# Kernel tuning notes

Measured on AMD Instinct MI355X. Metric: run time of the kernel, lower is better.

## Reference

```python
import jax, jax.numpy as jnp
import numpy as np

B = 512          # batch
V = 6890         # SMPL vertices
NB = 10          # num_betas
NJ = 24          # joints (root + 23 body)
# canonical SMPL kinematic tree (parents[0] = -1 for root)
PARENTS = np.array([-1,0,0,0,1,2,3,4,5,6,7,8,9,9,9,12,13,14,16,17,18,19,20,21], dtype=np.int32)


def rodrigues(rot_vecs):
    """Axis-angle [N,3] -> rotation matrices [N,3,3] (matches batch_rodrigues)."""
    angle = jnp.linalg.norm(rot_vecs + 1e-8, axis=1, keepdims=True)  # [N,1]
    rot_dir = rot_vecs / angle
    cos = jnp.cos(angle)[:, :, None]  # [N,1,1]
    sin = jnp.sin(angle)[:, :, None]
    rx, ry, rz = rot_dir[:, 0], rot_dir[:, 1], rot_dir[:, 2]
    zeros = jnp.zeros_like(rx)
    K = jnp.stack([zeros, -rz, ry,
                   rz, zeros, -rx,
                   -ry, rx, zeros], axis=1).reshape(-1, 3, 3)
    I = jnp.eye(3, dtype=rot_vecs.dtype)
    return I[None] + sin * K + (1.0 - cos) * jnp.matmul(K, K)


def setup_inputs() -> dict:
    key = jax.random.key(0)
    ks = jax.random.split(key, 8)
    betas = jnp.concatenate([jnp.ones((B, 1), jnp.float32),
                             0.5 * jax.random.normal(ks[0], (B, NB), jnp.float32)], axis=1)
    body_pose = 0.3 * jax.random.normal(ks[1], (B, 3 * (NJ - 1)), jnp.float32)
    global_orient = 0.3 * jax.random.normal(ks[2], (B, 3), jnp.float32)
    transl = jax.random.normal(ks[3], (B, 3), jnp.float32)
    shapedirs = 0.01 * jax.random.normal(ks[4], (V, 3, NB), jnp.float32)
    v_template = jax.random.normal(ks[5], (V, 3), jnp.float32)
    Jr = jax.random.uniform(ks[6], (NJ, V), jnp.float32)
    Jr = Jr / jnp.sum(Jr, axis=1, keepdims=True)
    W = jax.random.uniform(ks[7], (V, NJ), jnp.float32)
    W = W / jnp.sum(W, axis=1, keepdims=True)             # convex skinning weights
    return dict(betas=betas, body_pose=body_pose, global_orient=global_orient,
                transl=transl, shapedirs=shapedirs, v_template=v_template,
                J_regressor=Jr, lbs_weights=W)


def reference(betas, body_pose, global_orient, transl,
              shapedirs, v_template, J_regressor, lbs_weights):
    dt = v_template.dtype
    blend = jnp.einsum('bl,mkl->bmk', betas[:, 1:], shapedirs)            # [B,V,3]
    v_shaped = (v_template[None] + blend) * betas[:, 0][:, None, None]    # [B,V,3]
    J = jnp.einsum('bik,ji->bjk', v_shaped, J_regressor)                  # [B,NJ,3]
    # ---- updatePose: axis-angle -> rotmats
    full_pose = jnp.concatenate([global_orient, body_pose], axis=1)       # [B,NJ*3]
    rot_mats = rodrigues(full_pose.reshape(-1, 3)).reshape(-1, NJ, 3, 3)  # [B,NJ,3,3]
    # ---- kinematic chain (batch_rigid_transform)
    rel = J.at[:, 1:].add(-J[:, PARENTS[1:]])                             # rel joint offsets
    T_local = jnp.concatenate([rot_mats, rel[..., None]], axis=3)         # [B,NJ,3,4]
    bottom = jnp.broadcast_to(jnp.array([0, 0, 0, 1], dt), (rot_mats.shape[0], NJ, 1, 4))
    T_local = jnp.concatenate([T_local, bottom], axis=2)                  # [B,NJ,4,4]
    chain = [T_local[:, 0]]
    for i in range(1, NJ):  # fixed 24-node tree
        chain.append(jnp.matmul(chain[PARENTS[i]], T_local[:, i]))
    transforms = jnp.stack(chain, axis=1)                                 # [B,NJ,4,4]
    J_transformed = transforms[:, :, :3, 3]                               # [B,NJ,3]
    # relative transforms: subtract rotated rest joint from translation column
    init_t = jnp.einsum('bnij,bnj->bni', transforms[:, :, :3, :3], J)
    A = transforms.at[:, :, :3, 3].add(-init_t)                           # [B,NJ,4,4]
    # ---- skinning: T = W @ A, apply to homogeneous verts
    T = jnp.einsum('vn,bnij->bvij', lbs_weights, A)                       # [B,V,4,4]
    verts = (jnp.einsum('bvij,bvj->bvi', T[:, :, :3, :3], v_shaped)
             + T[:, :, :3, 3] + transl[:, None])                          # [B,V,3]
    return verts, J_transformed
```

## Files before the change

### kernel.cpp

```cpp
#include <hip/hip_runtime.h>

#define BATCH 512
#define V 6890
#define NJ 24
#define VH (V/2)

#define SD_N (V*30)
#define VT_N (V*3)
#define W_N  (V*24)
#define TOT_PK (SD_N+VT_N+W_N)

#define A_OFF   0
#define BS_OFF  147456
#define JT_OFF  155648
#define JS_OFF  155720
#define PK_OFF  156672

__device__ const int d_par[NJ] = {-1,0,0,0,1,2,3,4,5,6,7,8,9,9,9,12,13,14,16,17,18,19,20,21};

__global__ __launch_bounds__(256) void prep_k(
    const float* __restrict__ sd, const float* __restrict__ vt, const float* __restrict__ W,
    float* __restrict__ dst)
{
  int i = blockIdx.x*256 + threadIdx.x;
  if (i >= TOT_PK) return;
  float val;
  if (i < SD_N){ int j=i/V, v=i-j*V; val = sd[v*30+j]; }
  else if (i < SD_N+VT_N){ int o=i-SD_N; int j=o/V, v=o-j*V; val = vt[v*3+j]; }
  else { int o=i-SD_N-VT_N; int j=o/V, v=o-j*V; val = W[v*24+j]; }
  dst[i] = val;
}

__global__ __launch_bounds__(256) void jreg_k(
    const float* __restrict__ Jr, const float* __restrict__ pk,
    float* __restrict__ JTo, float* __restrict__ JSo)
{
  const int j = blockIdx.x;
  const int c = blockIdx.y;
  const int t = threadIdx.x;
  const float* __restrict__ col = (c<3) ? (pk + (30+c)*V) : (pk + (c-3)*V);
  float acc = 0.f;
  for (int v=t; v<V; v+=256){
    acc = fmaf(Jr[j*V+v], col[v], acc);
  }
  __shared__ float red[256];
  red[t]=acc; __syncthreads();
  for (int s=128;s>0;s>>=1){ if(t<s) red[t]+=red[t+s]; __syncthreads(); }
  if (t==0){
    if (c<3) JTo[j*3+c]=red[0];
    else {
      int idx=c-3, k=idx/10, l=idx-10*(idx/10);
      JSo[(j*3+k)*10+l] = red[0];
    }
  }
}

__global__ __launch_bounds__(64) void batch_k(
    const float* __restrict__ betas, const float* __restrict__ body_pose,
    const float* __restrict__ go, const float* __restrict__ transl,
    const float* __restrict__ JT, const float* __restrict__ JS,
    float* __restrict__ A, float* __restrict__ bsc, float* __restrict__ jout)
{
  const int b = blockIdx.x;
  const int t = threadIdx.x;
  __shared__ float lb[11];
  __shared__ float lJ[72];
  __shared__ float lR[NJ*9];
  __shared__ float lL[NJ*12];
  __shared__ float lW[NJ*12];
  if (t < 11) lb[t] = betas[b*11+t];
  __syncthreads();
  const float b0 = lb[0];
  for (int idx=t; idx<72; idx+=64){
    float s = JT[idx];
    #pragma unroll
    for (int l=0;l<10;l++) s = fmaf(lb[1+l], JS[idx*10+l], s);
    lJ[idx] = b0*s;
  }
  if (t==0) bsc[b*16] = b0;
  if (t>=1 && t<11) bsc[b*16+t] = b0*lb[t];
  if (t<3) bsc[b*16+11+t] = transl[b*3+t];
  if (t < NJ){
    float p0,p1,p2;
    if (t==0){ p0=go[b*3+0]; p1=go[b*3+1]; p2=go[b*3+2]; }
    else { int o=b*69+(t-1)*3; p0=body_pose[o]; p1=body_pose[o+1]; p2=body_pose[o+2]; }
    float a0=p0+1e-8f, a1=p1+1e-8f, a2=p2+1e-8f;
    float angle = sqrtf(a0*a0+a1*a1+a2*a2);
    float inv = 1.0f/angle;
    float rx=p0*inv, ry=p1*inv, rz=p2*inv;
    float sn = sinf(angle), cs = cosf(angle), mc = 1.0f-cs;
    float K[9] = {0.f,-rz,ry, rz,0.f,-rx, -ry,rx,0.f};
    float KK[9];
    #pragma unroll
    for (int r=0;r<3;r++)
      #pragma unroll
      for (int c=0;c<3;c++)
        KK[r*3+c] = K[r*3+0]*K[0+c] + K[r*3+1]*K[3+c] + K[r*3+2]*K[6+c];
    #pragma unroll
    for (int e=0;e<9;e++){
      float ident = (e==0||e==4||e==8)?1.0f:0.0f;
      lR[t*9+e] = ident + sn*K[e] + mc*KK[e];
    }
  }
  __syncthreads();
  for (int idx=t; idx<288; idx+=64){
    int j = idx/12, rc = idx-12*j, r = rc>>2, c = rc&3;
    float val;
    if (c<3) val = lR[j*9 + r*3 + c];
    else {
      int p = (j==0) ? 0 : d_par[j];
      val = (j==0) ? lJ[r] : (lJ[j*3+r] - lJ[p*3+r]);
    }
    lL[idx] = val;
  }
  __syncthreads();
  if (t<12) lW[t] = lL[t];
  __syncthreads();
  for (int i=1;i<NJ;i++){
    if (t<12){
      int p = d_par[i];
      int r = t>>2, c = t&3;
      float s = lW[p*12+r*4+0]*lL[i*12+0+c]
              + lW[p*12+r*4+1]*lL[i*12+4+c]
              + lW[p*12+r*4+2]*lL[i*12+8+c];
      if (c==3) s += lW[p*12+r*4+3];
      lW[i*12+t] = s;
    }
    __syncthreads();
  }
  for (int idx=t; idx<72; idx+=64){
    int j=idx/3, k=idx-3*j;
    jout[b*72+idx] = lW[j*12+k*4+3];
  }
  const int g = b>>2, q = b&3;
  float* __restrict__ Ab = A + g*1152 + q*12;
  for (int idx=t; idx<288; idx+=64){
    int n=idx/12, rc=idx-12*n, r=rc>>2, c=rc&3;
    float val = lW[n*12+rc];
    if (c==3){
      val -= lW[n*12+r*4+0]*lJ[n*3+0] + lW[n*12+r*4+1]*lJ[n*3+1] + lW[n*12+r*4+2]*lJ[n*3+2];
    }
    Ab[n*48 + rc] = val;
  }
}

__global__ __launch_bounds__(256) void main_k(
    const float* __restrict__ A, const float* __restrict__ bsc,
    const float2* __restrict__ pk, float* __restrict__ out)
{
  const int vh = blockIdx.x*256 + threadIdx.x;
  if (vh >= VH) return;
  const int bg = blockIdx.y;
  const float* __restrict__ Ag = A + bg*1152;
  const float* __restrict__ bs = bsc + bg*64;

  const float2 vt0 = pk[30*VH + vh];
  const float2 vt1 = pk[31*VH + vh];
  const float2 vt2 = pk[32*VH + vh];

  float2 vs[4][3];
#pragma unroll
  for (int q=0;q<4;q++){
    const float b0 = bs[q*16];
    vs[q][0] = make_float2(b0*vt0.x, b0*vt0.y);
    vs[q][1] = make_float2(b0*vt1.x, b0*vt1.y);
    vs[q][2] = make_float2(b0*vt2.x, b0*vt2.y);
  }
#pragma unroll
  for (int l=0;l<10;l++){
    const float2 s0 = pk[(0*10+l)*VH + vh];
    const float2 s1 = pk[(1*10+l)*VH + vh];
    const float2 s2 = pk[(2*10+l)*VH + vh];
#pragma unroll
    for (int q=0;q<4;q++){
      const float c = bs[q*16+1+l];
      vs[q][0].x = fmaf(c, s0.x, vs[q][0].x); vs[q][0].y = fmaf(c, s0.y, vs[q][0].y);
      vs[q][1].x = fmaf(c, s1.x, vs[q][1].x); vs[q][1].y = fmaf(c, s1.y, vs[q][1].y);
      vs[q][2].x = fmaf(c, s2.x, vs[q][2].x); vs[q][2].y = fmaf(c, s2.y, vs[q][2].y);
    }
  }

  float y[4][6];
#pragma unroll
  for (int q=0;q<4;q++)
#pragma unroll
    for (int i=0;i<6;i++) y[q][i] = 0.f;

#pragma unroll 4
  for (int n=0;n<NJ;n++){
    const float2 w = pk[(33+n)*VH + vh];
#pragma unroll
    for (int q=0;q<4;q++){
      const float* __restrict__ an = Ag + n*48 + q*12;
      float tt;
      tt = fmaf(an[2], vs[q][2].x, fmaf(an[1], vs[q][1].x, fmaf(an[0], vs[q][0].x, an[3])));
      y[q][0] = fmaf(w.x, tt, y[q][0]);
      tt = fmaf(an[2], vs[q][2].y, fmaf(an[1], vs[q][1].y, fmaf(an[0], vs[q][0].y, an[3])));
      y[q][1] = fmaf(w.y, tt, y[q][1]);
      tt = fmaf(an[6], vs[q][2].x, fmaf(an[5], vs[q][1].x, fmaf(an[4], vs[q][0].x, an[7])));
      y[q][2] = fmaf(w.x, tt, y[q][2]);
      tt = fmaf(an[6], vs[q][2].y, fmaf(an[5], vs[q][1].y, fmaf(an[4], vs[q][0].y, an[7])));
      y[q][3] = fmaf(w.y, tt, y[q][3]);
      tt = fmaf(an[10], vs[q][2].x, fmaf(an[9], vs[q][1].x, fmaf(an[8], vs[q][0].x, an[11])));
      y[q][4] = fmaf(w.x, tt, y[q][4]);
      tt = fmaf(an[10], vs[q][2].y, fmaf(an[9], vs[q][1].y, fmaf(an[8], vs[q][0].y, an[11])));
      y[q][5] = fmaf(w.y, tt, y[q][5]);
    }
  }

  const int v0 = 2*vh;
#pragma unroll
  for (int q=0;q<4;q++){
    const float t0 = bs[q*16+11], t1 = bs[q*16+12], t2 = bs[q*16+13];
    const int b = bg*4 + q;
    float2* __restrict__ o2 = (float2*)(out + (b*V + v0)*3);
    o2[0] = make_float2(y[q][0]+t0, y[q][2]+t1);
    o2[1] = make_float2(y[q][4]+t2, y[q][1]+t0);
    o2[2] = make_float2(y[q][3]+t1, y[q][5]+t2);
  }
}

extern "C" void kernel_launch(void* const* d_in, const int* in_sizes, int n_in,
                              void* d_out, int out_size, void* d_ws, size_t ws_size,
                              hipStream_t stream)
{
  const float* betas     = (const float*)d_in[0];
  const float* body_pose = (const float*)d_in[1];
  const float* go        = (const float*)d_in[2];
  const float* transl    = (const float*)d_in[3];
  const float* sdirs     = (const float*)d_in[4];
  const float* vtempl    = (const float*)d_in[5];
  const float* Jr        = (const float*)d_in[6];
  const float* lw        = (const float*)d_in[7];
  float* wsf = (float*)d_ws;
  float* out = (float*)d_out;

  hipLaunchKernelGGL(prep_k, dim3((TOT_PK+255)/256), dim3(256), 0, stream,
                     sdirs, vtempl, lw, wsf+PK_OFF);
  hipLaunchKernelGGL(jreg_k, dim3(24,33), dim3(256), 0, stream,
                     Jr, wsf+PK_OFF, wsf+JT_OFF, wsf+JS_OFF);
  hipLaunchKernelGGL(batch_k, dim3(BATCH), dim3(64), 0, stream,
                     betas, body_pose, go, transl, wsf+JT_OFF, wsf+JS_OFF,
                     wsf+A_OFF, wsf+BS_OFF, out + BATCH*V*3);
  hipLaunchKernelGGL(main_k, dim3((VH+255)/256, BATCH/4), dim3(256), 0, stream,
                     wsf+A_OFF, wsf+BS_OFF, (const float2*)(wsf+PK_OFF), out);
}
```

Measured before the change: 149.5 us.

## Fuse prep and joint regression, level-parallel kinematic chain, two vertex pairs per thread

Merges the weight-repacking kernel and the joint-regression kernel into one launch, with the regression reading the original strided inputs directly so it no longer waits on the repack. The serial 23-step kinematic chain in batch_k becomes 8 depth levels, where all joints at one level are computed in parallel, cutting barrier count. The main skinning kernel now processes two vertex pairs per thread so the per-joint A coefficients loaded from memory are reused across both. The trade-offs are more registers (possible occupancy loss), half as many blocks in main_k, and strided uncoalesced reads in the regression path.

New measurement: 237.0 us. +58.5%, slower.

```diff
diff --git a/kernel.cpp b/kernel.cpp
--- a/kernel.cpp
+++ b/kernel.cpp
@@ -9,6 +9,7 @@
 #define VT_N (V*3)
 #define W_N  (V*24)
 #define TOT_PK (SD_N+VT_N+W_N)
+#define PREP_BLOCKS ((TOT_PK+255)/256)
 
 #define A_OFF   0
 #define BS_OFF  147456
@@ -17,40 +18,44 @@
 #define PK_OFF  156672
 
 __device__ const int d_par[NJ] = {-1,0,0,0,1,2,3,4,5,6,7,8,9,9,9,12,13,14,16,17,18,19,20,21};
-
-__global__ __launch_bounds__(256) void prep_k(
-    const float* __restrict__ sd, const float* __restrict__ vt, const float* __restrict__ W,
-    float* __restrict__ dst)
-{
-  int i = blockIdx.x*256 + threadIdx.x;
-  if (i >= TOT_PK) return;
-  float val;
-  if (i < SD_N){ int j=i/V, v=i-j*V; val = sd[v*30+j]; }
-  else if (i < SD_N+VT_N){ int o=i-SD_N; int j=o/V, v=o-j*V; val = vt[v*3+j]; }
-  else { int o=i-SD_N-VT_N; int j=o/V, v=o-j*V; val = W[v*24+j]; }
-  dst[i] = val;
-}
-
-__global__ __launch_bounds__(256) void jreg_k(
-    const float* __restrict__ Jr, const float* __restrict__ pk,
-    float* __restrict__ JTo, float* __restrict__ JSo)
-{
-  const int j = blockIdx.x;
-  const int c = blockIdx.y;
+__device__ const int lvlJ[8][5] = {{1,2,3,0,0},{4,5,6,0,0},{7,8,9,0,0},{10,11,12,13,14},
+                                   {15,16,17,0,0},{18,19,0,0,0},{20,21,0,0,0},{22,23,0,0,0}};
+__device__ const int lvlP[8][5] = {{0,0,0,0,0},{1,2,3,0,0},{4,5,6,0,0},{7,8,9,9,9},
+                                   {12,13,14,0,0},{16,17,0,0,0},{18,19,0,0,0},{20,21,0,0,0}};
+__device__ const int lvlN[8] = {3,3,3,5,3,2,2,2};
+
+__global__ __launch_bounds__(256) void prepjr_k(
+    const float* __restrict__ sd, const float* __restrict__ vt,
+    const float* __restrict__ W, const float* __restrict__ Jr,
+    float* __restrict__ dst, float* __restrict__ JTo, float* __restrict__ JSo)
+{
+  const int bx = blockIdx.x;
   const int t = threadIdx.x;
-  const float* __restrict__ col = (c<3) ? (pk + (30+c)*V) : (pk + (c-3)*V);
-  float acc = 0.f;
-  for (int v=t; v<V; v+=256){
-    acc = fmaf(Jr[j*V+v], col[v], acc);
-  }
-  __shared__ float red[256];
-  red[t]=acc; __syncthreads();
-  for (int s=128;s>0;s>>=1){ if(t<s) red[t]+=red[t+s]; __syncthreads(); }
-  if (t==0){
-    if (c<3) JTo[j*3+c]=red[0];
-    else {
-      int idx=c-3, k=idx/10, l=idx-10*(idx/10);
-      JSo[(j*3+k)*10+l] = red[0];
+  if (bx < PREP_BLOCKS){
+    int i = bx*256 + t;
+    if (i >= TOT_PK) return;
+    float val;
+    if (i < SD_N){ int j=i/V, v=i-j*V; val = sd[v*30+j]; }
+    else if (i < SD_N+VT_N){ int o=i-SD_N; int j=o/V, v=o-j*V; val = vt[v*3+j]; }
+    else { int o=i-SD_N-VT_N; int j=o/V, v=o-j*V; val = W[v*24+j]; }
+    dst[i] = val;
+  } else {
+    const int idx = bx - PREP_BLOCKS;
+    const int j = idx/33, c = idx-33*(idx/33);
+    float acc = 0.f;
+    for (int v=t; v<V; v+=256){
+      float x = (c<3) ? vt[v*3+c] : sd[v*30+(c-3)];
+      acc = fmaf(Jr[j*V+v], x, acc);
+    }
+    __shared__ float red[256];
+    red[t]=acc; __syncthreads();
+    for (int s=128;s>0;s>>=1){ if(t<s) red[t]+=red[t+s]; __syncthreads(); }
+    if (t==0){
+      if (c<3) JTo[j*3+c]=red[0];
+      else {
+        int ii=c-3, k=ii/10, l=ii-10*(ii/10);
+        JSo[(j*3+k)*10+l] = red[0];
+      }
     }
   }
 }
@@ -116,15 +121,17 @@
   __syncthreads();
   if (t<12) lW[t] = lL[t];
   __syncthreads();
-  for (int i=1;i<NJ;i++){
-    if (t<12){
-      int p = d_par[i];
-      int r = t>>2, c = t&3;
-      float s = lW[p*12+r*4+0]*lL[i*12+0+c]
-              + lW[p*12+r*4+1]*lL[i*12+4+c]
-              + lW[p*12+r*4+2]*lL[i*12+8+c];
+  #pragma unroll
+  for (int lev=0; lev<8; lev++){
+    const int cnt = lvlN[lev];
+    if (t < cnt*12){
+      int jl = t/12, e = t-12*jl, r = e>>2, c = e&3;
+      int j = lvlJ[lev][jl], p = lvlP[lev][jl];
+      float s = lW[p*12+r*4+0]*lL[j*12+0+c]
+              + lW[p*12+r*4+1]*lL[j*12+4+c]
+              + lW[p*12+r*4+2]*lL[j*12+8+c];
       if (c==3) s += lW[p*12+r*4+3];
-      lW[i*12+t] = s;
+      lW[j*12+e] = s;
     }
     __syncthreads();
   }
@@ -148,75 +155,104 @@
     const float* __restrict__ A, const float* __restrict__ bsc,
     const float2* __restrict__ pk, float* __restrict__ out)
 {
-  const int vh = blockIdx.x*256 + threadIdx.x;
-  if (vh >= VH) return;
+  const int t = threadIdx.x;
+  const int p0 = blockIdx.x*512 + t;
+  if (p0 >= VH) return;
+  const int p1r = p0 + 256;
+  const bool has1 = (p1r < VH);
+  const int p1 = has1 ? p1r : p0;
   const int bg = blockIdx.y;
   const float* __restrict__ Ag = A + bg*1152;
   const float* __restrict__ bs = bsc + bg*64;
 
-  const float2 vt0 = pk[30*VH + vh];
-  const float2 vt1 = pk[31*VH + vh];
-  const float2 vt2 = pk[32*VH + vh];
-
-  float2 vs[4][3];
-#pragma unroll
-  for (int q=0;q<4;q++){
-    const float b0 = bs[q*16];
-    vs[q][0] = make_float2(b0*vt0.x, b0*vt0.y);
-    vs[q][1] = make_float2(b0*vt1.x, b0*vt1.y);
-    vs[q][2] = make_float2(b0*vt2.x, b0*vt2.y);
+  float2 va[4][3], vb[4][3];
+  {
+    const float2 t0a = pk[30*VH+p0], t0b = pk[30*VH+p1];
+    const float2 t1a = pk[31*VH+p0], t1b = pk[31*VH+p1];
+    const float2 t2a = pk[32*VH+p0], t2b = pk[32*VH+p1];
+#pragma unroll
+    for (int q=0;q<4;q++){
+      const float c0 = bs[q*16];
+      va[q][0]=make_float2(c0*t0a.x,c0*t0a.y); vb[q][0]=make_float2(c0*t0b.x,c0*t0b.y);
+      va[q][1]=make_float2(c0*t1a.x,c0*t1a.y); vb[q][1]=make_float2(c0*t1b.x,c0*t1b.y);
+      va[q][2]=make_float2(c0*t2a.x,c0*t2a.y); vb[q][2]=make_float2(c0*t2b.x,c0*t2b.y);
+    }
   }
 #pragma unroll
   for (int l=0;l<10;l++){
-    const float2 s0 = pk[(0*10+l)*VH + vh];
-    const float2 s1 = pk[(1*10+l)*VH + vh];
-    const float2 s2 = pk[(2*10+l)*VH + vh];
+    const float2 s0a = pk[l*VH+p0],      s0b = pk[l*VH+p1];
+    const float2 s1a = pk[(10+l)*VH+p0], s1b = pk[(10+l)*VH+p1];
+    const float2 s2a = pk[(20+l)*VH+p0], s2b = pk[(20+l)*VH+p1];
 #pragma unroll
     for (int q=0;q<4;q++){
       const float c = bs[q*16+1+l];
-      vs[q][0].x = fmaf(c, s0.x, vs[q][0].x); vs[q][0].y = fmaf(c, s0.y, vs[q][0].y);
-      vs[q][1].x = fmaf(c, s1.x, vs[q][1].x); vs[q][1].y = fmaf(c, s1.y, vs[q][1].y);
-      vs[q][2].x = fmaf(c, s2.x, vs[q][2].x); vs[q][2].y = fmaf(c, s2.y, vs[q][2].y);
-    }
-  }
-
-  float y[4][6];
+      va[q][0].x=fmaf(c,s0a.x,va[q][0].x); va[q][0].y=fmaf(c,s0a.y,va[q][0].y);
+      va[q][1].x=fmaf(c,s1a.x,va[q][1].x); va[q][1].y=fmaf(c,s1a.y,va[q][1].y);
+      va[q][2].x=fmaf(c,s2a.x,va[q][2].x); va[q][2].y=fmaf(c,s2a.y,va[q][2].y);
+      vb[q][0].x=fmaf(c,s0b.x,vb[q][0].x); vb[q][0].y=fmaf(c,s0b.y,vb[q][0].y);
+      vb[q][1].x=fmaf(c,s1b.x,vb[q][1].x); vb[q][1].y=fmaf(c,s1b.y,vb[q][1].y);
+      vb[q][2].x=fmaf(c,s2b.x,vb[q][2].x); vb[q][2].y=fmaf(c,s2b.y,vb[q][2].y);
+    }
+  }
+
+  float ya[4][6], yb[4][6];
 #pragma unroll
   for (int q=0;q<4;q++)
 #pragma unroll
-    for (int i=0;i<6;i++) y[q][i] = 0.f;
+    for (int i=0;i<6;i++){ ya[q][i]=0.f; yb[q][i]=0.f; }
 
 #pragma unroll 4
   for (int n=0;n<NJ;n++){
-    const float2 w = pk[(33+n)*VH + vh];
+    const float2 wa = pk[(33+n)*VH+p0];
+    const float2 wb = pk[(33+n)*VH+p1];
 #pragma unroll
     for (int q=0;q<4;q++){
       const float* __restrict__ an = Ag + n*48 + q*12;
       float tt;
-      tt = fmaf(an[2], vs[q][2].x, fmaf(an[1], vs[q][1].x, fmaf(an[0], vs[q][0].x, an[3])));
-      y[q][0] = fmaf(w.x, tt, y[q][0]);
-      tt = fmaf(an[2], vs[q][2].y, fmaf(an[1], vs[q][1].y, fmaf(an[0], vs[q][0].y, an[3])));
-      y[q][1] = fmaf(w.y, tt, y[q][1]);
-      tt = fmaf(an[6], vs[q][2].x, fmaf(an[5], vs[q][1].x, fmaf(an[4], vs[q][0].x, an[7])));
-      y[q][2] = fmaf(w.x, tt, y[q][2]);
-      tt = fmaf(an[6], vs[q][2].y, fmaf(an[5], vs[q][1].y, fmaf(an[4], vs[q][0].y, an[7])));
-      y[q][3] = fmaf(w.y, tt, y[q][3]);
-      tt = fmaf(an[10], vs[q][2].x, fmaf(an[9], vs[q][1].x, fmaf(an[8], vs[q][0].x, an[11])));
-      y[q][4] = fmaf(w.x, tt, y[q][4]);
-      tt = fmaf(an[10], vs[q][2].y, fmaf(an[9], vs[q][1].y, fmaf(an[8], vs[q][0].y, an[11])));
-      y[q][5] = fmaf(w.y, tt, y[q][5]);
-    }
-  }
-
-  const int v0 = 2*vh;
+      tt = fmaf(an[2], va[q][2].x, fmaf(an[1], va[q][1].x, fmaf(an[0], va[q][0].x, an[3])));
+      ya[q][0] = fmaf(wa.x, tt, ya[q][0]);
+      tt = fmaf(an[2], va[q][2].y, fmaf(an[1], va[q][1].y, fmaf(an[0], va[q][0].y, an[3])));
+      ya[q][1] = fmaf(wa.y, tt, ya[q][1]);
+      tt = fmaf(an[6], va[q][2].x, fmaf(an[5], va[q][1].x, fmaf(an[4], va[q][0].x, an[7])));
+      ya[q][2] = fmaf(wa.x, tt, ya[q][2]);
+      tt = fmaf(an[6], va[q][2].y, fmaf(an[5], va[q][1].y, fmaf(an[4], va[q][0].y, an[7])));
+      ya[q][3] = fmaf(wa.y, tt, ya[q][3]);
+      tt = fmaf(an[10], va[q][2].x, fmaf(an[9], va[q][1].x, fmaf(an[8], va[q][0].x, an[11])));
+      ya[q][4] = fmaf(wa.x, tt, ya[q][4]);
+      tt = fmaf(an[10], va[q][2].y, fmaf(an[9], va[q][1].y, fmaf(an[8], va[q][0].y, an[11])));
+      ya[q][5] = fmaf(wa.y, tt, ya[q][5]);
+
+      tt = fmaf(an[2], vb[q][2].x, fmaf(an[1], vb[q][1].x, fmaf(an[0], vb[q][0].x, an[3])));
+      yb[q][0] = fmaf(wb.x, tt, yb[q][0]);
+      tt = fmaf(an[2], vb[q][2].y, fmaf(an[1], vb[q][1].y, fmaf(an[0], vb[q][0].y, an[3])));
+      yb[q][1] = fmaf(wb.y, tt, yb[q][1]);
+      tt = fmaf(an[6], vb[q][2].x, fmaf(an[5], vb[q][1].x, fmaf(an[4], vb[q][0].x, an[7])));
+      yb[q][2] = fmaf(wb.x, tt, yb[q][2]);
+      tt = fmaf(an[6], vb[q][2].y, fmaf(an[5], vb[q][1].y, fmaf(an[4], vb[q][0].y, an[7])));
+      yb[q][3] = fmaf(wb.y, tt, yb[q][3]);
+      tt = fmaf(an[10], vb[q][2].x, fmaf(an[9], vb[q][1].x, fmaf(an[8], vb[q][0].x, an[11])));
+      yb[q][4] = fmaf(wb.x, tt, yb[q][4]);
+      tt = fmaf(an[10], vb[q][2].y, fmaf(an[9], vb[q][1].y, fmaf(an[8], vb[q][0].y, an[11])));
+      yb[q][5] = fmaf(wb.y, tt, yb[q][5]);
+    }
+  }
+
+  const int v0 = 2*p0;
+  const int v1 = 2*p1r;
 #pragma unroll
   for (int q=0;q<4;q++){
     const float t0 = bs[q*16+11], t1 = bs[q*16+12], t2 = bs[q*16+13];
     const int b = bg*4 + q;
-    float2* __restrict__ o2 = (float2*)(out + (b*V + v0)*3);
-    o2[0] = make_float2(y[q][0]+t0, y[q][2]+t1);
-    o2[1] = make_float2(y[q][4]+t2, y[q][1]+t0);
-    o2[2] = make_float2(y[q][3]+t1, y[q][5]+t2);
+    float2* __restrict__ oa = (float2*)(out + (b*V + v0)*3);
+    oa[0] = make_float2(ya[q][0]+t0, ya[q][2]+t1);
+    oa[1] = make_float2(ya[q][4]+t2, ya[q][1]+t0);
+    oa[2] = make_float2(ya[q][3]+t1, ya[q][5]+t2);
+    if (has1){
+      float2* __restrict__ ob = (float2*)(out + (b*V + v1)*3);
+      ob[0] = make_float2(yb[q][0]+t0, yb[q][2]+t1);
+      ob[1] = make_float2(yb[q][4]+t2, yb[q][1]+t0);
+      ob[2] = make_float2(yb[q][3]+t1, yb[q][5]+t2);
+    }
   }
 }
 
@@ -235,13 +271,11 @@
   float* wsf = (float*)d_ws;
   float* out = (float*)d_out;
 
-  hipLaunchKernelGGL(prep_k, dim3((TOT_PK+255)/256), dim3(256), 0, stream,
-                     sdirs, vtempl, lw, wsf+PK_OFF);
-  hipLaunchKernelGGL(jreg_k, dim3(24,33), dim3(256), 0, stream,
-                     Jr, wsf+PK_OFF, wsf+JT_OFF, wsf+JS_OFF);
+  hipLaunchKernelGGL(prepjr_k, dim3(PREP_BLOCKS + 24*33), dim3(256), 0, stream,
+                     sdirs, vtempl, lw, Jr, wsf+PK_OFF, wsf+JT_OFF, wsf+JS_OFF);
   hipLaunchKernelGGL(batch_k, dim3(BATCH), dim3(64), 0, stream,
                      betas, body_pose, go, transl, wsf+JT_OFF, wsf+JS_OFF,
                      wsf+A_OFF, wsf+BS_OFF, out + BATCH*V*3);
-  hipLaunchKernelGGL(main_k, dim3((VH+255)/256, BATCH/4), dim3(256), 0, stream,
+  hipLaunchKernelGGL(main_k, dim3((VH+511)/512, BATCH/4), dim3(256), 0, stream,
                      wsf+A_OFF, wsf+BS_OFF, (const float2*)(wsf+PK_OFF), out);
 }
```

## Merge prep and joint-regression kernels, level-parallel kinematic chain, preload skin weights

Applied to the files above, without the earlier changes.

Merges the transpose/pack kernel and the joint-regression kernel into one launch. The regression blocks now read the original strided shapedirs and template instead of waiting for the packed copy, which removes one launch and a dependency. In batch_k, the serial 23-step kinematic chain becomes 8 tree levels whose joints are computed in parallel, so there are fewer barriers. main_k preloads all 24 skin-weight pairs into registers up front and sets a launch-bounds occupancy hint of 4. The cost is higher register pressure and possible spilling, plus uncoalesced strided reads in the regression path.

Result: slower. 257.4 us (+72.2%).

```diff
diff --git a/kernel.cpp b/kernel.cpp
--- a/kernel.cpp
+++ b/kernel.cpp
@@ -9,6 +9,7 @@
 #define VT_N (V*3)
 #define W_N  (V*24)
 #define TOT_PK (SD_N+VT_N+W_N)
+#define PREP_BLOCKS ((TOT_PK+255)/256)
 
 #define A_OFF   0
 #define BS_OFF  147456
@@ -17,40 +18,44 @@
 #define PK_OFF  156672
 
 __device__ const int d_par[NJ] = {-1,0,0,0,1,2,3,4,5,6,7,8,9,9,9,12,13,14,16,17,18,19,20,21};
-
-__global__ __launch_bounds__(256) void prep_k(
-    const float* __restrict__ sd, const float* __restrict__ vt, const float* __restrict__ W,
-    float* __restrict__ dst)
-{
-  int i = blockIdx.x*256 + threadIdx.x;
-  if (i >= TOT_PK) return;
-  float val;
-  if (i < SD_N){ int j=i/V, v=i-j*V; val = sd[v*30+j]; }
-  else if (i < SD_N+VT_N){ int o=i-SD_N; int j=o/V, v=o-j*V; val = vt[v*3+j]; }
-  else { int o=i-SD_N-VT_N; int j=o/V, v=o-j*V; val = W[v*24+j]; }
-  dst[i] = val;
-}
-
-__global__ __launch_bounds__(256) void jreg_k(
-    const float* __restrict__ Jr, const float* __restrict__ pk,
-    float* __restrict__ JTo, float* __restrict__ JSo)
-{
-  const int j = blockIdx.x;
-  const int c = blockIdx.y;
+__device__ const int lvlJ[8][5] = {{1,2,3,0,0},{4,5,6,0,0},{7,8,9,0,0},{10,11,12,13,14},
+                                   {15,16,17,0,0},{18,19,0,0,0},{20,21,0,0,0},{22,23,0,0,0}};
+__device__ const int lvlP[8][5] = {{0,0,0,0,0},{1,2,3,0,0},{4,5,6,0,0},{7,8,9,9,9},
+                                   {12,13,14,0,0},{16,17,0,0,0},{18,19,0,0,0},{20,21,0,0,0}};
+__device__ const int lvlN[8] = {3,3,3,5,3,2,2,2};
+
+__global__ __launch_bounds__(256) void prepjr_k(
+    const float* __restrict__ sd, const float* __restrict__ vt,
+    const float* __restrict__ W, const float* __restrict__ Jr,
+    float* __restrict__ dst, float* __restrict__ JTo, float* __restrict__ JSo)
+{
+  const int bx = blockIdx.x;
   const int t = threadIdx.x;
-  const float* __restrict__ col = (c<3) ? (pk + (30+c)*V) : (pk + (c-3)*V);
-  float acc = 0.f;
-  for (int v=t; v<V; v+=256){
-    acc = fmaf(Jr[j*V+v], col[v], acc);
-  }
-  __shared__ float red[256];
-  red[t]=acc; __syncthreads();
-  for (int s=128;s>0;s>>=1){ if(t<s) red[t]+=red[t+s]; __syncthreads(); }
-  if (t==0){
-    if (c<3) JTo[j*3+c]=red[0];
-    else {
-      int idx=c-3, k=idx/10, l=idx-10*(idx/10);
-      JSo[(j*3+k)*10+l] = red[0];
+  if (bx < PREP_BLOCKS){
+    int i = bx*256 + t;
+    if (i >= TOT_PK) return;
+    float val;
+    if (i < SD_N){ int j=i/V, v=i-j*V; val = sd[v*30+j]; }
+    else if (i < SD_N+VT_N){ int o=i-SD_N; int j=o/V, v=o-j*V; val = vt[v*3+j]; }
+    else { int o=i-SD_N-VT_N; int j=o/V, v=o-j*V; val = W[v*24+j]; }
+    dst[i] = val;
+  } else {
+    const int idx = bx - PREP_BLOCKS;
+    const int j = idx/33, c = idx-33*(idx/33);
+    float acc = 0.f;
+    for (int v=t; v<V; v+=256){
+      float x = (c<3) ? vt[v*3+c] : sd[v*30+(c-3)];
+      acc = fmaf(Jr[j*V+v], x, acc);
+    }
+    __shared__ float red[256];
+    red[t]=acc; __syncthreads();
+    for (int s=128;s>0;s>>=1){ if(t<s) red[t]+=red[t+s]; __syncthreads(); }
+    if (t==0){
+      if (c<3) JTo[j*3+c]=red[0];
+      else {
+        int ii=c-3, k=ii/10, l=ii-10*(ii/10);
+        JSo[(j*3+k)*10+l] = red[0];
+      }
     }
   }
 }
@@ -116,15 +121,17 @@
   __syncthreads();
   if (t<12) lW[t] = lL[t];
   __syncthreads();
-  for (int i=1;i<NJ;i++){
-    if (t<12){
-      int p = d_par[i];
-      int r = t>>2, c = t&3;
-      float s = lW[p*12+r*4+0]*lL[i*12+0+c]
-              + lW[p*12+r*4+1]*lL[i*12+4+c]
-              + lW[p*12+r*4+2]*lL[i*12+8+c];
+  #pragma unroll
+  for (int lev=0; lev<8; lev++){
+    const int cnt = lvlN[lev];
+    if (t < cnt*12){
+      int jl = t/12, e = t-12*jl, r = e>>2, c = e&3;
+      int j = lvlJ[lev][jl], p = lvlP[lev][jl];
+      float s = lW[p*12+r*4+0]*lL[j*12+0+c]
+              + lW[p*12+r*4+1]*lL[j*12+4+c]
+              + lW[p*12+r*4+2]*lL[j*12+8+c];
       if (c==3) s += lW[p*12+r*4+3];
-      lW[i*12+t] = s;
+      lW[j*12+e] = s;
     }
     __syncthreads();
   }
@@ -144,7 +151,7 @@
   }
 }
 
-__global__ __launch_bounds__(256) void main_k(
+__global__ __launch_bounds__(256, 4) void main_k(
     const float* __restrict__ A, const float* __restrict__ bsc,
     const float2* __restrict__ pk, float* __restrict__ out)
 {
@@ -154,6 +161,10 @@
   const float* __restrict__ Ag = A + bg*1152;
   const float* __restrict__ bs = bsc + bg*64;
 
+  float2 w[NJ];
+#pragma unroll
+  for (int n=0;n<NJ;n++) w[n] = pk[(33+n)*VH + vh];
+
   const float2 vt0 = pk[30*VH + vh];
   const float2 vt1 = pk[31*VH + vh];
   const float2 vt2 = pk[32*VH + vh];
@@ -168,9 +179,9 @@
   }
 #pragma unroll
   for (int l=0;l<10;l++){
-    const float2 s0 = pk[(0*10+l)*VH + vh];
-    const float2 s1 = pk[(1*10+l)*VH + vh];
-    const float2 s2 = pk[(2*10+l)*VH + vh];
+    const float2 s0 = pk[l*VH + vh];
+    const float2 s1 = pk[(10+l)*VH + vh];
+    const float2 s2 = pk[(20+l)*VH + vh];
 #pragma unroll
     for (int q=0;q<4;q++){
       const float c = bs[q*16+1+l];
@@ -188,23 +199,23 @@
 
 #pragma unroll 4
   for (int n=0;n<NJ;n++){
-    const float2 w = pk[(33+n)*VH + vh];
+    const float wx = w[n].x, wy = w[n].y;
 #pragma unroll
     for (int q=0;q<4;q++){
       const float* __restrict__ an = Ag + n*48 + q*12;
       float tt;
       tt = fmaf(an[2], vs[q][2].x, fmaf(an[1], vs[q][1].x, fmaf(an[0], vs[q][0].x, an[3])));
-      y[q][0] = fmaf(w.x, tt, y[q][0]);
+      y[q][0] = fmaf(wx, tt, y[q][0]);
       tt = fmaf(an[2], vs[q][2].y, fmaf(an[1], vs[q][1].y, fmaf(an[0], vs[q][0].y, an[3])));
-      y[q][1] = fmaf(w.y, tt, y[q][1]);
+      y[q][1] = fmaf(wy, tt, y[q][1]);
       tt = fmaf(an[6], vs[q][2].x, fmaf(an[5], vs[q][1].x, fmaf(an[4], vs[q][0].x, an[7])));
-      y[q][2] = fmaf(w.x, tt, y[q][2]);
+      y[q][2] = fmaf(wx, tt, y[q][2]);
       tt = fmaf(an[6], vs[q][2].y, fmaf(an[5], vs[q][1].y, fmaf(an[4], vs[q][0].y, an[7])));
-      y[q][3] = fmaf(w.y, tt, y[q][3]);
+      y[q][3] = fmaf(wy, tt, y[q][3]);
       tt = fmaf(an[10], vs[q][2].x, fmaf(an[9], vs[q][1].x, fmaf(an[8], vs[q][0].x, an[11])));
-      y[q][4] = fmaf(w.x, tt, y[q][4]);
+      y[q][4] = fmaf(wx, tt, y[q][4]);
       tt = fmaf(an[10], vs[q][2].y, fmaf(an[9], vs[q][1].y, fmaf(an[8], vs[q][0].y, an[11])));
-      y[q][5] = fmaf(w.y, tt, y[q][5]);
+      y[q][5] = fmaf(wy, tt, y[q][5]);
     }
   }
 
@@ -235,10 +246,8 @@
   float* wsf = (float*)d_ws;
   float* out = (float*)d_out;
 
-  hipLaunchKernelGGL(prep_k, dim3((TOT_PK+255)/256), dim3(256), 0, stream,
-                     sdirs, vtempl, lw, wsf+PK_OFF);
-  hipLaunchKernelGGL(jreg_k, dim3(24,33), dim3(256), 0, stream,
-                     Jr, wsf+PK_OFF, wsf+JT_OFF, wsf+JS_OFF);
+  hipLaunchKernelGGL(prepjr_k, dim3(PREP_BLOCKS + 24*33), dim3(256), 0, stream,
+                     sdirs, vtempl, lw, Jr, wsf+PK_OFF, wsf+JT_OFF, wsf+JS_OFF);
   hipLaunchKernelGGL(batch_k, dim3(BATCH), dim3(64), 0, stream,
                      betas, body_pose, go, transl, wsf+JT_OFF, wsf+JS_OFF,
                      wsf+A_OFF, wsf+BS_OFF, out + BATCH*V*3);
```
